# Performance work log

Measured on AMD Instinct MI355X. Metric: run time of the kernel, lower is better.

## Reference

```python
import jax, jax.numpy as jnp
import numpy as np

D, DK, DV, H = 1024, 64, 1024, 16
DVH = DV // H  # per-head value dim
EPS = 1e-5


def _layer_norm(x, g, b):
    mu = jnp.mean(x, axis=-1, keepdims=True)
    var = jnp.var(x, axis=-1, keepdims=True)
    return (x - mu) * jax.lax.rsqrt(var + EPS) * g + b


def setup_inputs() -> dict:
    key = jax.random.key(0)
    ks = jax.random.split(key, 12)
    s = lambda k, shape, fan_in: jax.random.normal(k, shape, jnp.float32) / np.sqrt(fan_in)
    return {
        "x": jax.random.normal(ks[0], (2, 2048, D), jnp.float32),
        "Wq": s(ks[1], (H, D, DK), D),
        "Wk": s(ks[2], (H, D, DK), D),
        "Wv": s(ks[3], (H, D, DVH), D),
        "Wo": s(ks[4], (DV, D), DV),
        "ln1_g": jnp.ones((D,), jnp.float32),
        "ln1_b": jnp.zeros((D,), jnp.float32),
        "W1": s(ks[5], (D, 4 * D), D),
        "b1": jnp.zeros((4 * D,), jnp.float32),
        "W2": s(ks[6], (4 * D, D), 4 * D),
        "b2": jnp.zeros((D,), jnp.float32),
        "ln2_g": jnp.ones((D,), jnp.float32),
        "ln2_b": jnp.zeros((D,), jnp.float32),
    }


def reference(x, Wq, Wk, Wv, Wo, ln1_g, ln1_b, W1, b1, W2, b2, ln2_g, ln2_b):
    B, S, _ = x.shape
    # per-head projections (vectorized over the head loop of the original)
    q = jnp.einsum("bsd,hdk->bhsk", x, Wq)
    k = jnp.einsum("bsd,hdk->bhsk", x, Wk)
    v = jnp.einsum("bsd,hdv->bhsv", x, Wv)
    scores = jnp.einsum("bhsk,bhtk->bhst", q, k) / np.sqrt(DK).astype(np.float32)
    attn = jax.nn.softmax(scores, axis=-1)
    o = jnp.einsum("bhst,bhtv->bhsv", attn, v)  # [B,H,S,DVH]
    o = o.transpose(0, 2, 1, 3).reshape(B, S, DV)  # concat heads
    attn_out = o @ Wo
    x1 = _layer_norm(attn_out + x, ln1_g, ln1_b)
    ffn = jax.nn.relu(x1 @ W1 + b1) @ W2 + b2
    return _layer_norm(ffn + x1, ln2_g, ln2_b)
```

## Files before the change

### kernel.cpp

```cpp
#include <hip/hip_runtime.h>
#include <hip/hip_bf16.h>

typedef unsigned short u16;
typedef unsigned int u32;
typedef short short8 __attribute__((ext_vector_type(8)));
typedef float fx4 __attribute__((ext_vector_type(4)));

__device__ __forceinline__ float b2f(u16 x) {
  return __uint_as_float(((u32)x) << 16);
}
__device__ __forceinline__ u16 f2b(float f) {
  u32 u = __float_as_uint(f);
  u += 0x7fffu + ((u >> 16) & 1u);
  return (u16)(u >> 16);
}

__device__ __forceinline__ void load16(const u16* g, u16* l) {
  __builtin_amdgcn_global_load_lds(
      (__attribute__((address_space(1))) void*)(u16*)g,
      (__attribute__((address_space(3))) void*)l, 16, 0, 0);
}

__global__ __launch_bounds__(256) void cvt_f2b_kernel(
    const float* __restrict__ in, u16* __restrict__ out)
{
  int i = (blockIdx.x * 256 + threadIdx.x) * 4;
  fx4 v = *(const fx4*)(in + i);
  u16 o4[4];
#pragma unroll
  for (int j = 0; j < 4; ++j) o4[j] = f2b(v[j]);
  *(uint2*)(out + i) = *(uint2*)o4;
}

__global__ __launch_bounds__(256) void transpose_f2b_kernel(
    const float* __restrict__ in, u16* __restrict__ out,
    int R, int C, int out_ld)
{
  __shared__ __align__(16) u16 tile[32][33];
  int tx = threadIdx.x, ty = threadIdx.y;
  int c0 = blockIdx.x * 32, r0 = blockIdx.y * 32;
  const float* inb = in + (size_t)blockIdx.z * R * C;
  u16* outb = out + (size_t)blockIdx.z * C * out_ld;
#pragma unroll
  for (int i = 0; i < 4; ++i)
    tile[ty + i * 8][tx] = f2b(inb[(size_t)(r0 + ty + i * 8) * C + c0 + tx]);
  __syncthreads();
#pragma unroll
  for (int i = 0; i < 4; ++i)
    outb[(size_t)(c0 + ty + i * 8) * out_ld + r0 + tx] = tile[tx][ty + i * 8];
}

__global__ __launch_bounds__(256) void transpose_b2b_kernel(
    const u16* __restrict__ in, u16* __restrict__ out, int in_ld, int out_ld)
{
  __shared__ __align__(16) u16 tile[32][33];
  int tx = threadIdx.x, ty = threadIdx.y;
  int c0 = blockIdx.x * 32, r0 = blockIdx.y * 32;
#pragma unroll
  for (int i = 0; i < 4; ++i)
    tile[ty + i * 8][tx] = in[(size_t)(r0 + ty + i * 8) * in_ld + c0 + tx];
  __syncthreads();
#pragma unroll
  for (int i = 0; i < 4; ++i)
    out[(size_t)(c0 + ty + i * 8) * out_ld + r0 + tx] = tile[tx][ty + i * 8];
}

__global__ __launch_bounds__(256, 2) void gemm_bt(
    const u16* __restrict__ A, const u16* __restrict__ BT,
    const float* __restrict__ bias, void* __restrict__ Cp,
    int M, int N, int K, int flags)
{
  __shared__ __align__(16) u16 As[2][4096];
  __shared__ __align__(16) u16 Bs[2][4096];
  int tid = threadIdx.x;
  int lane = tid & 63, wid = tid >> 6;
  int l15 = lane & 15, quad = lane >> 4;
  int wm = wid >> 1, wn = wid & 1;
  int m0 = blockIdx.y * 128, n0 = blockIdx.x * 128;

  int srow = wid * 16 + (lane >> 2);
  int sswz = (((lane >> 2) & 3) + ((lane >> 4) & 3)) & 3;
  int gch = (lane & 3) ^ sswz;
  const u16* gA = A + (size_t)(m0 + srow) * K + gch * 8;
  const u16* gB = BT + (size_t)(n0 + srow) * K + gch * 8;
  size_t gstep = (size_t)64 * K;
  u16* lA = &As[0][wid * 512];
  u16* lB = &Bs[0][wid * 512];

  int rswz = ((l15 & 3) + (l15 >> 2)) & 3;
  int rphys = ((quad ^ rswz) & 3) << 3;

  fx4 acc[4][4];
#pragma unroll
  for (int i = 0; i < 4; ++i)
#pragma unroll
    for (int j = 0; j < 4; ++j) acc[i][j] = fx4{0.f, 0.f, 0.f, 0.f};

  int nt = K >> 5;
  load16(gA,         lA);
  load16(gA + gstep, lA + 2048);
  load16(gB,         lB);
  load16(gB + gstep, lB + 2048);

  for (int kt = 0; kt < nt; ++kt) {
    __syncthreads();
    if (kt + 1 < nt) {
      int buf = (kt + 1) & 1;
      const u16* ga = gA + (kt + 1) * 32;
      const u16* gb = gB + (kt + 1) * 32;
      load16(ga,         lA + buf * 4096);
      load16(ga + gstep, lA + buf * 4096 + 2048);
      load16(gb,         lB + buf * 4096);
      load16(gb + gstep, lB + buf * 4096 + 2048);
    }
    const u16* Ab = As[kt & 1];
    const u16* Bb = Bs[kt & 1];
    short8 af[4], bf[4];
#pragma unroll
    for (int t = 0; t < 4; ++t)
      af[t] = *(const short8*)&Ab[(wm * 64 + t * 16 + l15) * 32 + rphys];
#pragma unroll
    for (int t = 0; t < 4; ++t)
      bf[t] = *(const short8*)&Bb[(wn * 64 + t * 16 + l15) * 32 + rphys];
#pragma unroll
    for (int tm = 0; tm < 4; ++tm)
#pragma unroll
      for (int tn = 0; tn < 4; ++tn)
        acc[tm][tn] = __builtin_amdgcn_mfma_f32_16x16x32_bf16(
            af[tm], bf[tn], acc[tm][tn], 0, 0, 0);
  }

  bool obf = flags & 1, hb = flags & 2, rl = flags & 4;
#pragma unroll
  for (int tn = 0; tn < 4; ++tn) {
    int col = n0 + wn * 64 + tn * 16 + l15;
    float bv = hb ? bias[col] : 0.0f;
#pragma unroll
    for (int tm = 0; tm < 4; ++tm) {
      int row = m0 + wm * 64 + tm * 16 + (quad << 2);
#pragma unroll
      for (int r = 0; r < 4; ++r) {
        float v = acc[tm][tn][r] + bv;
        if (rl) v = fmaxf(v, 0.0f);
        size_t idx = (size_t)(row + r) * N + col;
        if (obf) ((u16*)Cp)[idx] = f2b(v);
        else ((float*)Cp)[idx] = v;
      }
    }
  }
}

__global__ __launch_bounds__(256, 2) void gemm_bt_n64(
    const u16* __restrict__ A, const u16* __restrict__ BT,
    const float* __restrict__ bias, void* __restrict__ Cp,
    int M, int N, int K, int flags)
{
  __shared__ __align__(16) u16 As[2][4096];
  __shared__ __align__(16) u16 Bs[2][2048];
  int tid = threadIdx.x;
  int lane = tid & 63, wid = tid >> 6;
  int l15 = lane & 15, quad = lane >> 4;
  int wm = wid >> 1, wn = wid & 1;
  int m0 = blockIdx.y * 128, n0 = blockIdx.x * 64;
  int zz = blockIdx.z;
  int kc = K / (int)gridDim.z;

  int srow = wid * 16 + (lane >> 2);
  int sswz = (((lane >> 2) & 3) + ((lane >> 4) & 3)) & 3;
  int gch = (lane & 3) ^ sswz;
  const u16* gA = A + (size_t)(m0 + srow) * K + zz * kc + gch * 8;
  const u16* gB = BT + (size_t)(n0 + srow) * K + zz * kc + gch * 8;
  size_t gstep = (size_t)64 * K;
  u16* lA = &As[0][wid * 512];
  u16* lB = &Bs[0][wid * 512];

  int rswz = ((l15 & 3) + (l15 >> 2)) & 3;
  int rphys = ((quad ^ rswz) & 3) << 3;

  fx4 acc[4][2];
#pragma unroll
  for (int i = 0; i < 4; ++i)
#pragma unroll
    for (int j = 0; j < 2; ++j) acc[i][j] = fx4{0.f, 0.f, 0.f, 0.f};

  int nt = kc >> 5;
  load16(gA,         lA);
  load16(gA + gstep, lA + 2048);
  load16(gB,         lB);

  for (int kt = 0; kt < nt; ++kt) {
    __syncthreads();
    if (kt + 1 < nt) {
      int buf = (kt + 1) & 1;
      const u16* ga = gA + (kt + 1) * 32;
      const u16* gb = gB + (kt + 1) * 32;
      load16(ga,         lA + buf * 4096);
      load16(ga + gstep, lA + buf * 4096 + 2048);
      load16(gb,         lB + buf * 2048);
    }
    const u16* Ab = As[kt & 1];
    const u16* Bb = Bs[kt & 1];
    short8 af[4], bf[2];
#pragma unroll
    for (int t = 0; t < 4; ++t)
      af[t] = *(const short8*)&Ab[(wm * 64 + t * 16 + l15) * 32 + rphys];
#pragma unroll
    for (int t = 0; t < 2; ++t)
      bf[t] = *(const short8*)&Bb[(wn * 32 + t * 16 + l15) * 32 + rphys];
#pragma unroll
    for (int tm = 0; tm < 4; ++tm)
#pragma unroll
      for (int tn = 0; tn < 2; ++tn)
        acc[tm][tn] = __builtin_amdgcn_mfma_f32_16x16x32_bf16(
            af[tm], bf[tn], acc[tm][tn], 0, 0, 0);
  }

  bool obf = flags & 1, hb = flags & 2, rl = flags & 4;
  u16* cb16 = (u16*)Cp + (size_t)zz * M * N;
  float* cf32 = (float*)Cp + (size_t)zz * M * N;
#pragma unroll
  for (int tn = 0; tn < 2; ++tn) {
    int col = n0 + wn * 32 + tn * 16 + l15;
    float bv = hb ? bias[col] : 0.0f;
#pragma unroll
    for (int tm = 0; tm < 4; ++tm) {
      int row = m0 + wm * 64 + tm * 16 + (quad << 2);
#pragma unroll
      for (int r = 0; r < 4; ++r) {
        float v = acc[tm][tn][r] + bv;
        if (rl) v = fmaxf(v, 0.0f);
        size_t idx = (size_t)(row + r) * N + col;
        if (obf) cb16[idx] = f2b(v);
        else cf32[idx] = v;
      }
    }
  }
}

__global__ __launch_bounds__(256) void attn_kernel(
    const u16* __restrict__ qkv, const u16* __restrict__ vT,
    u16* __restrict__ o)
{
  __shared__ __align__(16) u16 Ks[2][4096];
  __shared__ __align__(16) u16 Vs[2][4096];
  __shared__ __align__(16) u16 Pw[4][1024];
  int tid = threadIdx.x;
  int lane = tid & 63, wid = tid >> 6;
  int l15 = lane & 15, quad = lane >> 4;
  int b = blockIdx.z, h = blockIdx.y;
  int q0 = blockIdx.x * 64 + wid * 16;

  const u16* qb = qkv + (size_t)(b * 2048 + q0 + l15) * 3072 + h * 64 + (quad << 3);
  short8 qf0 = *(const short8*)qb;
  short8 qf1 = *(const short8*)(qb + 32);

  int srow = tid >> 3;
  int gc8 = ((tid & 7) ^ (srow & 7)) << 3;
  const u16* kg = qkv + (size_t)(b * 2048 + srow) * 3072 + 1024 + h * 64 + gc8;
  const u16* vg = vT + (size_t)(h * 64 + srow) * 4096 + b * 2048 + gc8;
  u16* lk = &Ks[0][wid * 512];
  u16* lv = &Vs[0][wid * 512];

  const short8 kOnes = {0x3F80, 0x3F80, 0x3F80, 0x3F80,
                        0x3F80, 0x3F80, 0x3F80, 0x3F80};

  fx4 oacc[4];
  fx4 accl = fx4{0.f, 0.f, 0.f, 0.f};
#pragma unroll
  for (int i = 0; i < 4; ++i) oacc[i] = fx4{0.f, 0.f, 0.f, 0.f};

  load16(kg,             lk);
  load16(kg + 32 * 3072, lk + 2048);
  load16(vg,             lv);
  load16(vg + 32 * 4096, lv + 2048);

  int swz = l15 & 7;
  for (int kt = 0; kt < 32; ++kt) {
    __syncthreads();
    if (kt + 1 < 32) {
      int buf = (kt + 1) & 1;
      const u16* kgn = kg + (size_t)(kt + 1) * 64 * 3072;
      const u16* vgn = vg + (kt + 1) * 64;
      load16(kgn,             lk + buf * 4096);
      load16(kgn + 32 * 3072, lk + buf * 4096 + 2048);
      load16(vgn,             lv + buf * 4096);
      load16(vgn + 32 * 4096, lv + buf * 4096 + 2048);
    }
    const u16* Kb = Ks[kt & 1];
    const u16* Vb = Vs[kt & 1];

    fx4 sc[4];
#pragma unroll
    for (int sub = 0; sub < 4; ++sub) {
      sc[sub] = fx4{0.f, 0.f, 0.f, 0.f};
      const u16* rp = &Kb[(sub * 16 + l15) * 64];
      short8 kf0 = *(const short8*)&rp[((quad ^ swz) & 7) << 3];
      short8 kf1 = *(const short8*)&rp[(((4 | quad) ^ swz) & 7) << 3];
      sc[sub] = __builtin_amdgcn_mfma_f32_16x16x32_bf16(qf0, kf0, sc[sub], 0, 0, 0);
      sc[sub] = __builtin_amdgcn_mfma_f32_16x16x32_bf16(qf1, kf1, sc[sub], 0, 0, 0);
    }
#pragma unroll
    for (int sub = 0; sub < 4; ++sub) {
      int t = sub * 16 + l15;
#pragma unroll
      for (int r = 0; r < 4; ++r) {
        float p = __expf(sc[sub][r] * 0.125f);
        int q = (quad << 2) + r;
        int col = ((((t >> 3) ^ (q & 7)) & 7) << 3) | (t & 7);
        Pw[wid][(q << 6) | col] = f2b(p);
      }
    }
    short8 pf0 = *(const short8*)&Pw[wid][(l15 << 6) | (((quad ^ swz) & 7) << 3)];
    short8 pf1 = *(const short8*)&Pw[wid][(l15 << 6) | ((((4 | quad) ^ swz) & 7) << 3)];
    accl = __builtin_amdgcn_mfma_f32_16x16x32_bf16(pf0, kOnes, accl, 0, 0, 0);
    accl = __builtin_amdgcn_mfma_f32_16x16x32_bf16(pf1, kOnes, accl, 0, 0, 0);
#pragma unroll
    for (int dt = 0; dt < 4; ++dt) {
      const u16* rp = &Vb[(dt * 16 + l15) * 64];
      short8 vf0 = *(const short8*)&rp[((quad ^ swz) & 7) << 3];
      short8 vf1 = *(const short8*)&rp[(((4 | quad) ^ swz) & 7) << 3];
      oacc[dt] = __builtin_amdgcn_mfma_f32_16x16x32_bf16(pf0, vf0, oacc[dt], 0, 0, 0);
      oacc[dt] = __builtin_amdgcn_mfma_f32_16x16x32_bf16(pf1, vf1, oacc[dt], 0, 0, 0);
    }
  }
  fx4 inv;
#pragma unroll
  for (int r = 0; r < 4; ++r) inv[r] = 1.0f / accl[r];
#pragma unroll
  for (int dt = 0; dt < 4; ++dt) {
    int col = h * 64 + dt * 16 + l15;
#pragma unroll
    for (int r = 0; r < 4; ++r)
      o[(size_t)(b * 2048 + q0 + (quad << 2) + r) * 1024 + col] =
          f2b(oacc[dt][r] * inv[r]);
  }
}

__global__ __launch_bounds__(256) void ln_kernel(
    const float* __restrict__ main0, const float* __restrict__ main1,
    const float* __restrict__ res, const float* __restrict__ cbias,
    const float* __restrict__ g, const float* __restrict__ beta,
    u16* __restrict__ out_b, float* __restrict__ out_f)
{
  __shared__ float red[8];
  int row = blockIdx.x, tid = threadIdx.x;
  size_t base = (size_t)row * 1024 + tid * 4;
  fx4 v = *(const fx4*)(main0 + base);
  fx4 v1 = *(const fx4*)(main1 + base);
  fx4 rv = *(const fx4*)(res + base);
#pragma unroll
  for (int i = 0; i < 4; ++i) v[i] += v1[i] + rv[i];
  if (cbias) {
    fx4 cb = *(const fx4*)(cbias + tid * 4);
#pragma unroll
    for (int i = 0; i < 4; ++i) v[i] += cb[i];
  }
  float s = v[0] + v[1] + v[2] + v[3];
  float sq = v[0] * v[0] + v[1] * v[1] + v[2] * v[2] + v[3] * v[3];
#pragma unroll
  for (int off = 32; off >= 1; off >>= 1) {
    s += __shfl_xor(s, off, 64);
    sq += __shfl_xor(sq, off, 64);
  }
  int wid = tid >> 6, lane = tid & 63;
  if (lane == 0) { red[wid] = s; red[wid + 4] = sq; }
  __syncthreads();
  float S = red[0] + red[1] + red[2] + red[3];
  float SQ = red[4] + red[5] + red[6] + red[7];
  float mean = S * (1.0f / 1024.0f);
  float var = SQ * (1.0f / 1024.0f) - mean * mean;
  float rs = rsqrtf(var + 1e-5f);
  fx4 gv = *(const fx4*)(g + tid * 4);
  fx4 bv = *(const fx4*)(beta + tid * 4);
  float of[4];
#pragma unroll
  for (int i = 0; i < 4; ++i) of[i] = (v[i] - mean) * rs * gv[i] + bv[i];
  if (out_f) *(fx4*)(out_f + base) = *(const fx4*)of;
  if (out_b) {
    u16 o4[4];
#pragma unroll
    for (int i = 0; i < 4; ++i) o4[i] = f2b(of[i]);
    *(uint2*)(out_b + base) = *(uint2*)o4;
  }
}

extern "C" void kernel_launch(void* const* d_in, const int* in_sizes, int n_in,
                              void* d_out, int out_size, void* d_ws, size_t ws_size,
                              hipStream_t stream) {
  (void)in_sizes; (void)n_in; (void)out_size; (void)ws_size;
  const float* x     = (const float*)d_in[0];
  const float* Wq    = (const float*)d_in[1];
  const float* Wk    = (const float*)d_in[2];
  const float* Wv    = (const float*)d_in[3];
  const float* Wo    = (const float*)d_in[4];
  const float* g1    = (const float*)d_in[5];
  const float* bb1   = (const float*)d_in[6];
  const float* W1    = (const float*)d_in[7];
  const float* bias1 = (const float*)d_in[8];
  const float* W2    = (const float*)d_in[9];
  const float* bias2 = (const float*)d_in[10];
  const float* g2    = (const float*)d_in[11];
  const float* bb2   = (const float*)d_in[12];

  char* ws = (char*)d_ws;
  const size_t MB = 1048576;
  u16* xb     = (u16*)(ws);
  u16* wqkvT  = (u16*)(ws + 8 * MB);
  u16* woT    = (u16*)(ws + 38 * MB);
  u16* qkv    = (u16*)(ws + 40 * MB);
  u16* vT     = (u16*)(ws + 64 * MB);
  u16* ob     = (u16*)(ws + 72 * MB);
  float* aout = (float*)(ws);
  u16* x1     = (u16*)(ws + 64 * MB);
  float* x1f  = (float*)(ws + 40 * MB);
  u16* w1T    = (u16*)(ws + 56 * MB);
  u16* w2T    = (u16*)(ws);
  u16* hbuf   = (u16*)(ws + 8 * MB);
  float* ffn  = (float*)(ws + 56 * MB);

  dim3 tb(32, 8, 1);
  cvt_f2b_kernel<<<4096, 256, 0, stream>>>(x, xb);
  transpose_f2b_kernel<<<dim3(2, 32, 16), tb, 0, stream>>>(Wq, wqkvT,           1024, 64, 1024);
  transpose_f2b_kernel<<<dim3(2, 32, 16), tb, 0, stream>>>(Wk, wqkvT + 1048576, 1024, 64, 1024);
  transpose_f2b_kernel<<<dim3(2, 32, 16), tb, 0, stream>>>(Wv, wqkvT + 2097152, 1024, 64, 1024);
  transpose_f2b_kernel<<<dim3(32, 32, 1), tb, 0, stream>>>(Wo, woT, 1024, 1024, 1024);

  gemm_bt<<<dim3(24, 32), 256, 0, stream>>>(xb, wqkvT, nullptr, qkv, 4096, 3072, 1024, 1);
  transpose_b2b_kernel<<<dim3(32, 128), tb, 0, stream>>>(qkv + 2048, vT, 3072, 4096);
  attn_kernel<<<dim3(32, 16, 2), 256, 0, stream>>>(qkv, vT, ob);
  gemm_bt_n64<<<dim3(16, 32, 2), 256, 0, stream>>>(ob, woT, nullptr, aout, 4096, 1024, 1024, 0);
  ln_kernel<<<4096, 256, 0, stream>>>(aout, aout + 4194304, x, nullptr, g1, bb1, x1, x1f);
  transpose_f2b_kernel<<<dim3(128, 32, 1), tb, 0, stream>>>(W1, w1T, 1024, 4096, 1024);
  transpose_f2b_kernel<<<dim3(32, 128, 1), tb, 0, stream>>>(W2, w2T, 4096, 1024, 4096);
  gemm_bt<<<dim3(32, 32), 256, 0, stream>>>(x1, w1T, bias1, hbuf, 4096, 4096, 1024, 1 | 2 | 4);
  gemm_bt_n64<<<dim3(16, 32, 2), 256, 0, stream>>>(hbuf, w2T, nullptr, ffn, 4096, 1024, 4096, 0);
  ln_kernel<<<4096, 256, 0, stream>>>(ffn, ffn + 4194304, x1f, bias2, g2, bb2, nullptr, (float*)d_out);
}
```

Before: 399.2 us.

## Keep attention probabilities in registers via transposed QK MFMA, drop LDS round-trip

Swaps the MFMA operand order for QK^T so each lane holds scores for one query across key positions. The packed bf16 probabilities can then feed the PV MFMA directly as the A operand without going through LDS. The V reads are reshuffled to match the permuted key ordering. The row sum moves from a ones-matrix MFMA to per-lane adds plus cross-lane shuffles. This removes LDS writes and reads of P and two MFMAs per tile, at the cost of narrower 8-byte V loads from LDS.

```diff
diff --git a/kernel.cpp b/kernel.cpp
--- a/kernel.cpp
+++ b/kernel.cpp
@@ -5,6 +5,7 @@
 typedef unsigned int u32;
 typedef short short8 __attribute__((ext_vector_type(8)));
 typedef float fx4 __attribute__((ext_vector_type(4)));
+typedef u32 ux4 __attribute__((ext_vector_type(4)));
 
 __device__ __forceinline__ float b2f(u16 x) {
   return __uint_as_float(((u32)x) << 16);
@@ -13,6 +14,11 @@
   u32 u = __float_as_uint(f);
   u += 0x7fffu + ((u >> 16) & 1u);
   return (u16)(u >> 16);
+}
+__device__ __forceinline__ u32 cvtpk(float a, float b) {
+  u32 r;
+  asm("v_cvt_pk_bf16_f32 %0, %1, %2" : "=v"(r) : "v"(a), "v"(b));
+  return r;
 }
 
 __device__ __forceinline__ void load16(const u16* g, u16* l) {
@@ -243,7 +249,6 @@
 {
   __shared__ __align__(16) u16 Ks[2][4096];
   __shared__ __align__(16) u16 Vs[2][4096];
-  __shared__ __align__(16) u16 Pw[4][1024];
   int tid = threadIdx.x;
   int lane = tid & 63, wid = tid >> 6;
   int l15 = lane & 15, quad = lane >> 4;
@@ -261,11 +266,8 @@
   u16* lk = &Ks[0][wid * 512];
   u16* lv = &Vs[0][wid * 512];
 
-  const short8 kOnes = {0x3F80, 0x3F80, 0x3F80, 0x3F80,
-                        0x3F80, 0x3F80, 0x3F80, 0x3F80};
-
   fx4 oacc[4];
-  fx4 accl = fx4{0.f, 0.f, 0.f, 0.f};
+  float suml = 0.0f;
 #pragma unroll
   for (int i = 0; i < 4; ++i) oacc[i] = fx4{0.f, 0.f, 0.f, 0.f};
 
@@ -275,6 +277,8 @@
   load16(vg + 32 * 4096, lv + 2048);
 
   int swz = l15 & 7;
+  int q2 = quad >> 1;
+  int h4 = (quad & 1) * 4;
   for (int kt = 0; kt < 32; ++kt) {
     __syncthreads();
     if (kt + 1 < 32) {
@@ -296,36 +300,45 @@
       const u16* rp = &Kb[(sub * 16 + l15) * 64];
       short8 kf0 = *(const short8*)&rp[((quad ^ swz) & 7) << 3];
       short8 kf1 = *(const short8*)&rp[(((4 | quad) ^ swz) & 7) << 3];
-      sc[sub] = __builtin_amdgcn_mfma_f32_16x16x32_bf16(qf0, kf0, sc[sub], 0, 0, 0);
-      sc[sub] = __builtin_amdgcn_mfma_f32_16x16x32_bf16(qf1, kf1, sc[sub], 0, 0, 0);
-    }
+      sc[sub] = __builtin_amdgcn_mfma_f32_16x16x32_bf16(kf0, qf0, sc[sub], 0, 0, 0);
+      sc[sub] = __builtin_amdgcn_mfma_f32_16x16x32_bf16(kf1, qf1, sc[sub], 0, 0, 0);
+    }
+
+    u32 W[4][2];
+    float ps = 0.0f;
 #pragma unroll
     for (int sub = 0; sub < 4; ++sub) {
-      int t = sub * 16 + l15;
-#pragma unroll
-      for (int r = 0; r < 4; ++r) {
-        float p = __expf(sc[sub][r] * 0.125f);
-        int q = (quad << 2) + r;
-        int col = ((((t >> 3) ^ (q & 7)) & 7) << 3) | (t & 7);
-        Pw[wid][(q << 6) | col] = f2b(p);
-      }
-    }
-    short8 pf0 = *(const short8*)&Pw[wid][(l15 << 6) | (((quad ^ swz) & 7) << 3)];
-    short8 pf1 = *(const short8*)&Pw[wid][(l15 << 6) | ((((4 | quad) ^ swz) & 7) << 3)];
-    accl = __builtin_amdgcn_mfma_f32_16x16x32_bf16(pf0, kOnes, accl, 0, 0, 0);
-    accl = __builtin_amdgcn_mfma_f32_16x16x32_bf16(pf1, kOnes, accl, 0, 0, 0);
+      float p0 = __expf(sc[sub][0] * 0.125f);
+      float p1 = __expf(sc[sub][1] * 0.125f);
+      float p2 = __expf(sc[sub][2] * 0.125f);
+      float p3 = __expf(sc[sub][3] * 0.125f);
+      ps += (p0 + p1) + (p2 + p3);
+      W[sub][0] = cvtpk(p0, p1);
+      W[sub][1] = cvtpk(p2, p3);
+    }
+    suml += ps;
+    short8 pa1 = __builtin_bit_cast(short8, ux4{W[0][0], W[0][1], W[1][0], W[1][1]});
+    short8 pa2 = __builtin_bit_cast(short8, ux4{W[2][0], W[2][1], W[3][0], W[3][1]});
+
 #pragma unroll
     for (int dt = 0; dt < 4; ++dt) {
       const u16* rp = &Vb[(dt * 16 + l15) * 64];
-      short8 vf0 = *(const short8*)&rp[((quad ^ swz) & 7) << 3];
-      short8 vf1 = *(const short8*)&rp[(((4 | quad) ^ swz) & 7) << 3];
-      oacc[dt] = __builtin_amdgcn_mfma_f32_16x16x32_bf16(pf0, vf0, oacc[dt], 0, 0, 0);
-      oacc[dt] = __builtin_amdgcn_mfma_f32_16x16x32_bf16(pf1, vf1, oacc[dt], 0, 0, 0);
-    }
-  }
+      uint2 v0a = *(const uint2*)&rp[(((q2)     ^ swz) << 3) + h4];
+      uint2 v0b = *(const uint2*)&rp[(((2 + q2) ^ swz) << 3) + h4];
+      uint2 v1a = *(const uint2*)&rp[(((4 + q2) ^ swz) << 3) + h4];
+      uint2 v1b = *(const uint2*)&rp[(((6 + q2) ^ swz) << 3) + h4];
+      short8 vf0 = __builtin_bit_cast(short8, ux4{v0a.x, v0a.y, v0b.x, v0b.y});
+      short8 vf1 = __builtin_bit_cast(short8, ux4{v1a.x, v1a.y, v1b.x, v1b.y});
+      oacc[dt] = __builtin_amdgcn_mfma_f32_16x16x32_bf16(pa1, vf0, oacc[dt], 0, 0, 0);
+      oacc[dt] = __builtin_amdgcn_mfma_f32_16x16x32_bf16(pa2, vf1, oacc[dt], 0, 0, 0);
+    }
+  }
+  suml += __shfl_xor(suml, 16, 64);
+  suml += __shfl_xor(suml, 32, 64);
   fx4 inv;
 #pragma unroll
-  for (int r = 0; r < 4; ++r) inv[r] = 1.0f / accl[r];
+  for (int r = 0; r < 4; ++r)
+    inv[r] = 1.0f / __shfl(suml, (quad << 2) + r, 64);
 #pragma unroll
   for (int dt = 0; dt < 4; ++dt) {
     int col = h * 64 + dt * 16 + l15;
```

Result: no change. 402.9 us (+0.9%).

## Keep attention probabilities in registers and double query rows per wave

Applied to the files above, without the earlier changes.

The attention kernel now computes transposed scores (K as the A operand) so that the exp'd probabilities, packed with v_cvt_pk_bf16_f32 and rearranged via permlane32_swap, can feed the PV MFMA straight from registers. This removes the per-tile LDS round-trip through the Pw buffer and the ones-vector MFMA for the row sums. Row sums are kept as scalar partials and reduced with shuffles at the end. Each wave now handles 32 query rows instead of 16, reusing every K/V fragment twice and halving the grid, with exp2 using a prescaled constant and setprio around the MFMA blocks. The cost is more registers per thread and a dependence on a non-obvious row permutation being correct.

```diff
diff --git a/kernel.cpp b/kernel.cpp
--- a/kernel.cpp
+++ b/kernel.cpp
@@ -5,6 +5,8 @@
 typedef unsigned int u32;
 typedef short short8 __attribute__((ext_vector_type(8)));
 typedef float fx4 __attribute__((ext_vector_type(4)));
+typedef u32 ux4 __attribute__((ext_vector_type(4)));
+typedef u32 ux2 __attribute__((ext_vector_type(2)));
 
 __device__ __forceinline__ float b2f(u16 x) {
   return __uint_as_float(((u32)x) << 16);
@@ -13,6 +15,11 @@
   u32 u = __float_as_uint(f);
   u += 0x7fffu + ((u >> 16) & 1u);
   return (u16)(u >> 16);
+}
+__device__ __forceinline__ u32 cvtpk(float a, float b) {
+  u32 r;
+  asm("v_cvt_pk_bf16_f32 %0, %1, %2" : "=v"(r) : "v"(a), "v"(b));
+  return r;
 }
 
 __device__ __forceinline__ void load16(const u16* g, u16* l) {
@@ -237,22 +244,24 @@
   }
 }
 
-__global__ __launch_bounds__(256) void attn_kernel(
+__global__ __launch_bounds__(256, 2) void attn_kernel(
     const u16* __restrict__ qkv, const u16* __restrict__ vT,
     u16* __restrict__ o)
 {
   __shared__ __align__(16) u16 Ks[2][4096];
   __shared__ __align__(16) u16 Vs[2][4096];
-  __shared__ __align__(16) u16 Pw[4][1024];
   int tid = threadIdx.x;
   int lane = tid & 63, wid = tid >> 6;
   int l15 = lane & 15, quad = lane >> 4;
   int b = blockIdx.z, h = blockIdx.y;
-  int q0 = blockIdx.x * 64 + wid * 16;
-
-  const u16* qb = qkv + (size_t)(b * 2048 + q0 + l15) * 3072 + h * 64 + (quad << 3);
-  short8 qf0 = *(const short8*)qb;
-  short8 qf1 = *(const short8*)(qb + 32);
+  int q0 = blockIdx.x * 128 + wid * 32;
+
+  const u16* qbA = qkv + (size_t)(b * 2048 + q0 + l15) * 3072 + h * 64 + (quad << 3);
+  short8 qA0 = *(const short8*)qbA;
+  short8 qA1 = *(const short8*)(qbA + 32);
+  const u16* qbB = qbA + (size_t)16 * 3072;
+  short8 qB0 = *(const short8*)qbB;
+  short8 qB1 = *(const short8*)(qbB + 32);
 
   int srow = tid >> 3;
   int gc8 = ((tid & 7) ^ (srow & 7)) << 3;
@@ -261,13 +270,17 @@
   u16* lk = &Ks[0][wid * 512];
   u16* lv = &Vs[0][wid * 512];
 
-  const short8 kOnes = {0x3F80, 0x3F80, 0x3F80, 0x3F80,
-                        0x3F80, 0x3F80, 0x3F80, 0x3F80};
-
-  fx4 oacc[4];
-  fx4 accl = fx4{0.f, 0.f, 0.f, 0.f};
-#pragma unroll
-  for (int i = 0; i < 4; ++i) oacc[i] = fx4{0.f, 0.f, 0.f, 0.f};
+  int lq = l15 >> 2;
+  int rs = ((((lq & 1) << 1) | (lq >> 1)) << 2) | (l15 & 3);
+  int sk = rs & 7;
+
+  fx4 oaccA[4], oaccB[4];
+  float sumA = 0.0f, sumB = 0.0f;
+#pragma unroll
+  for (int i = 0; i < 4; ++i) {
+    oaccA[i] = fx4{0.f, 0.f, 0.f, 0.f};
+    oaccB[i] = fx4{0.f, 0.f, 0.f, 0.f};
+  }
 
   load16(kg,             lk);
   load16(kg + 32 * 3072, lk + 2048);
@@ -275,6 +288,7 @@
   load16(vg + 32 * 4096, lv + 2048);
 
   int swz = l15 & 7;
+  const float SC = 0.18033688011112042f;
   for (int kt = 0; kt < 32; ++kt) {
     __syncthreads();
     if (kt + 1 < 32) {
@@ -289,50 +303,89 @@
     const u16* Kb = Ks[kt & 1];
     const u16* Vb = Vs[kt & 1];
 
-    fx4 sc[4];
+    fx4 scA[4], scB[4];
+    __builtin_amdgcn_s_setprio(1);
 #pragma unroll
     for (int sub = 0; sub < 4; ++sub) {
-      sc[sub] = fx4{0.f, 0.f, 0.f, 0.f};
-      const u16* rp = &Kb[(sub * 16 + l15) * 64];
-      short8 kf0 = *(const short8*)&rp[((quad ^ swz) & 7) << 3];
-      short8 kf1 = *(const short8*)&rp[(((4 | quad) ^ swz) & 7) << 3];
-      sc[sub] = __builtin_amdgcn_mfma_f32_16x16x32_bf16(qf0, kf0, sc[sub], 0, 0, 0);
-      sc[sub] = __builtin_amdgcn_mfma_f32_16x16x32_bf16(qf1, kf1, sc[sub], 0, 0, 0);
-    }
+      const u16* rp = &Kb[(sub * 16 + rs) * 64];
+      short8 kf0 = *(const short8*)&rp[((quad ^ sk) & 7) << 3];
+      short8 kf1 = *(const short8*)&rp[(((4 | quad) ^ sk) & 7) << 3];
+      scA[sub] = fx4{0.f, 0.f, 0.f, 0.f};
+      scA[sub] = __builtin_amdgcn_mfma_f32_16x16x32_bf16(kf0, qA0, scA[sub], 0, 0, 0);
+      scA[sub] = __builtin_amdgcn_mfma_f32_16x16x32_bf16(kf1, qA1, scA[sub], 0, 0, 0);
+      scB[sub] = fx4{0.f, 0.f, 0.f, 0.f};
+      scB[sub] = __builtin_amdgcn_mfma_f32_16x16x32_bf16(kf0, qB0, scB[sub], 0, 0, 0);
+      scB[sub] = __builtin_amdgcn_mfma_f32_16x16x32_bf16(kf1, qB1, scB[sub], 0, 0, 0);
+    }
+    __builtin_amdgcn_s_setprio(0);
+
+    u32 WA[4][2], WB[4][2];
+    float psA = 0.0f, psB = 0.0f;
 #pragma unroll
     for (int sub = 0; sub < 4; ++sub) {
-      int t = sub * 16 + l15;
-#pragma unroll
-      for (int r = 0; r < 4; ++r) {
-        float p = __expf(sc[sub][r] * 0.125f);
-        int q = (quad << 2) + r;
-        int col = ((((t >> 3) ^ (q & 7)) & 7) << 3) | (t & 7);
-        Pw[wid][(q << 6) | col] = f2b(p);
-      }
-    }
-    short8 pf0 = *(const short8*)&Pw[wid][(l15 << 6) | (((quad ^ swz) & 7) << 3)];
-    short8 pf1 = *(const short8*)&Pw[wid][(l15 << 6) | ((((4 | quad) ^ swz) & 7) << 3)];
-    accl = __builtin_amdgcn_mfma_f32_16x16x32_bf16(pf0, kOnes, accl, 0, 0, 0);
-    accl = __builtin_amdgcn_mfma_f32_16x16x32_bf16(pf1, kOnes, accl, 0, 0, 0);
+      float a0 = __builtin_amdgcn_exp2f(scA[sub][0] * SC);
+      float a1 = __builtin_amdgcn_exp2f(scA[sub][1] * SC);
+      float a2 = __builtin_amdgcn_exp2f(scA[sub][2] * SC);
+      float a3 = __builtin_amdgcn_exp2f(scA[sub][3] * SC);
+      psA += (a0 + a1) + (a2 + a3);
+      WA[sub][0] = cvtpk(a0, a1);
+      WA[sub][1] = cvtpk(a2, a3);
+      float b0 = __builtin_amdgcn_exp2f(scB[sub][0] * SC);
+      float b1 = __builtin_amdgcn_exp2f(scB[sub][1] * SC);
+      float b2 = __builtin_amdgcn_exp2f(scB[sub][2] * SC);
+      float b3 = __builtin_amdgcn_exp2f(scB[sub][3] * SC);
+      psB += (b0 + b1) + (b2 + b3);
+      WB[sub][0] = cvtpk(b0, b1);
+      WB[sub][1] = cvtpk(b2, b3);
+    }
+    sumA += psA;
+    sumB += psB;
+
+    ux2 eA00 = __builtin_amdgcn_permlane32_swap(WA[0][0], WA[1][0], false, false);
+    ux2 eA01 = __builtin_amdgcn_permlane32_swap(WA[0][1], WA[1][1], false, false);
+    ux2 eA10 = __builtin_amdgcn_permlane32_swap(WA[2][0], WA[3][0], false, false);
+    ux2 eA11 = __builtin_amdgcn_permlane32_swap(WA[2][1], WA[3][1], false, false);
+    short8 pa1A = __builtin_bit_cast(short8, ux4{eA00[0], eA01[0], eA00[1], eA01[1]});
+    short8 pa2A = __builtin_bit_cast(short8, ux4{eA10[0], eA11[0], eA10[1], eA11[1]});
+    ux2 eB00 = __builtin_amdgcn_permlane32_swap(WB[0][0], WB[1][0], false, false);
+    ux2 eB01 = __builtin_amdgcn_permlane32_swap(WB[0][1], WB[1][1], false, false);
+    ux2 eB10 = __builtin_amdgcn_permlane32_swap(WB[2][0], WB[3][0], false, false);
+    ux2 eB11 = __builtin_amdgcn_permlane32_swap(WB[2][1], WB[3][1], false, false);
+    short8 pa1B = __builtin_bit_cast(short8, ux4{eB00[0], eB01[0], eB00[1], eB01[1]});
+    short8 pa2B = __builtin_bit_cast(short8, ux4{eB10[0], eB11[0], eB10[1], eB11[1]});
+
+    __builtin_amdgcn_s_setprio(1);
 #pragma unroll
     for (int dt = 0; dt < 4; ++dt) {
       const u16* rp = &Vb[(dt * 16 + l15) * 64];
       short8 vf0 = *(const short8*)&rp[((quad ^ swz) & 7) << 3];
       short8 vf1 = *(const short8*)&rp[(((4 | quad) ^ swz) & 7) << 3];
-      oacc[dt] = __builtin_amdgcn_mfma_f32_16x16x32_bf16(pf0, vf0, oacc[dt], 0, 0, 0);
-      oacc[dt] = __builtin_amdgcn_mfma_f32_16x16x32_bf16(pf1, vf1, oacc[dt], 0, 0, 0);
-    }
-  }
-  fx4 inv;
-#pragma unroll
-  for (int r = 0; r < 4; ++r) inv[r] = 1.0f / accl[r];
+      oaccA[dt] = __builtin_amdgcn_mfma_f32_16x16x32_bf16(pa1A, vf0, oaccA[dt], 0, 0, 0);
+      oaccA[dt] = __builtin_amdgcn_mfma_f32_16x16x32_bf16(pa2A, vf1, oaccA[dt], 0, 0, 0);
+      oaccB[dt] = __builtin_amdgcn_mfma_f32_16x16x32_bf16(pa1B, vf0, oaccB[dt], 0, 0, 0);
+      oaccB[dt] = __builtin_amdgcn_mfma_f32_16x16x32_bf16(pa2B, vf1, oaccB[dt], 0, 0, 0);
+    }
+    __builtin_amdgcn_s_setprio(0);
+  }
+  sumA += __shfl_xor(sumA, 16, 64);
+  sumA += __shfl_xor(sumA, 32, 64);
+  sumB += __shfl_xor(sumB, 16, 64);
+  sumB += __shfl_xor(sumB, 32, 64);
+  fx4 invA, invB;
+#pragma unroll
+  for (int r = 0; r < 4; ++r) {
+    invA[r] = 1.0f / __shfl(sumA, (quad << 2) + r, 64);
+    invB[r] = 1.0f / __shfl(sumB, (quad << 2) + r, 64);
+  }
 #pragma unroll
   for (int dt = 0; dt < 4; ++dt) {
     int col = h * 64 + dt * 16 + l15;
 #pragma unroll
-    for (int r = 0; r < 4; ++r)
-      o[(size_t)(b * 2048 + q0 + (quad << 2) + r) * 1024 + col] =
-          f2b(oacc[dt][r] * inv[r]);
+    for (int r = 0; r < 4; ++r) {
+      size_t rowA = (size_t)(b * 2048 + q0 + (quad << 2) + r);
+      o[rowA * 1024 + col] = f2b(oaccA[dt][r] * invA[r]);
+      o[(rowA + 16) * 1024 + col] = f2b(oaccB[dt][r] * invB[r]);
+    }
   }
 }
 
@@ -427,7 +480,7 @@
 
   gemm_bt<<<dim3(24, 32), 256, 0, stream>>>(xb, wqkvT, nullptr, qkv, 4096, 3072, 1024, 1);
   transpose_b2b_kernel<<<dim3(32, 128), tb, 0, stream>>>(qkv + 2048, vT, 3072, 4096);
-  attn_kernel<<<dim3(32, 16, 2), 256, 0, stream>>>(qkv, vT, ob);
+  attn_kernel<<<dim3(16, 16, 2), 256, 0, stream>>>(qkv, vT, ob);
   gemm_bt_n64<<<dim3(16, 32, 2), 256, 0, stream>>>(ob, woT, nullptr, aout, 4096, 1024, 1024, 0);
   ln_kernel<<<4096, 256, 0, stream>>>(aout, aout + 4194304, x, nullptr, g1, bb1, x1, x1f);
   transpose_f2b_kernel<<<dim3(128, 32, 1), tb, 0, stream>>>(W1, w1T, 1024, 4096, 1024);
```

After: 381.8 us. -4.3%, faster.
